# Optimization experiments

Hardware: AMD Instinct MI355X
Metric: run time of the kernel (lower is better)

## Reference

```python
import jax, jax.numpy as jnp
import numpy as np
import math

NUM_HEADS = 3
WINDOW = 7


def _shift_masks(ws):
    # row_mask: block mask for windows wrapping across the bottom edge
    half = ws * (ws // 2)  # 21 for ws=7
    row = np.zeros((ws * ws, ws * ws), np.float32)
    row[-half:, :-half] = -np.inf
    row[:-half, -half:] = -np.inf
    # column_mask = rearrange(row, '(r w1) (c w2) -> (w1 r) (w2 c)')
    col = row.reshape(ws, ws, ws, ws).transpose(1, 0, 3, 2).reshape(ws * ws, ws * ws)
    return jnp.asarray(row), jnp.asarray(col)


def setup_inputs() -> dict:
    key = jax.random.key(0)
    ks = jax.random.split(key, 5)
    B, S, E = 64, 3136, 96
    return {
        'x': jax.random.normal(ks[0], (B, S, E), jnp.float32),
        'w1': jax.random.normal(ks[1], (3 * E, E), jnp.float32) * 0.05,
        'b1': jax.random.normal(ks[2], (3 * E,), jnp.float32) * 0.05,
        'w2': jax.random.normal(ks[3], (E, E), jnp.float32) * 0.05,
        'b2': jax.random.normal(ks[4], (E,), jnp.float32) * 0.05,
    }


def reference(x, w1, b1, w2, b2):
    b, S, E = x.shape
    h = w = int(math.sqrt(S))          # 56
    ws = WINDOW
    H = NUM_HEADS
    Eh = E // H                        # head dim = 32
    nh, nw = h // ws, w // ws          # windows per axis = 8
    scale = 1.0 / math.sqrt(E / H)
    # faithful to original: forward shift = -ws//2 = -4, inverse shift = ws//2 = 3
    shift_fwd = -ws // 2
    shift_bwd = ws // 2

    qkv = x @ w1.T + b1                              # [b, S, 3E]
    qkv = qkv.reshape(b, h, w, E, 3)                 # (c K) split, K fastest
    qkv = jnp.roll(qkv, (shift_fwd, shift_fwd), axis=(1, 2))
    # b (nh m1) (nw m2) (H Eh) K -> b H nh nw (m1 m2) Eh K
    qkv = qkv.reshape(b, nh, ws, nw, ws, H, Eh, 3)
    qkv = qkv.transpose(0, 5, 1, 3, 2, 4, 6, 7).reshape(b, H, nh, nw, ws * ws, Eh, 3)
    Q, K, V = qkv[..., 0], qkv[..., 1], qkv[..., 2]

    s = jnp.einsum('bHhwme,bHhwne->bHhwmn', Q, K) * scale  # [b,H,nh,nw,49,49]
    row_mask, col_mask = _shift_masks(ws)
    s = s.at[:, :, -1, :].add(row_mask)   # last row of windows
    s = s.at[:, :, :, -1].add(col_mask)   # last column of windows

    att = jax.nn.softmax(s, axis=-1)
    o = jnp.einsum('bHhwmn,bHhwne->bHhwme', att, V)        # [b,H,nh,nw,49,Eh]
    # b H nh nw (m1 m2) Eh -> b (nh m1) (nw m2) (H Eh)
    o = o.reshape(b, H, nh, nw, ws, ws, Eh)
    o = o.transpose(0, 2, 4, 3, 5, 1, 6).reshape(b, h, w, E)
    o = jnp.roll(o, (shift_bwd, shift_bwd), axis=(1, 2))
    o = o.reshape(b, S, E)
    return o @ w2.T + b2
```

## Files before the change

### kernel.cpp

```cpp
#include <hip/hip_runtime.h>


typedef _Float16 f16;
typedef _Float16 f16x2 __attribute__((ext_vector_type(2)));
typedef _Float16 f16x4 __attribute__((ext_vector_type(4)));
typedef _Float16 f16x8 __attribute__((ext_vector_type(8)));
typedef float f32x4 __attribute__((ext_vector_type(4)));

static __device__ __forceinline__ f32x4 mfma16(f16x8 a, f16x8 b, f32x4 c) {
    return __builtin_amdgcn_mfma_f32_16x16x32_f16(a, b, c, 0, 0, 0);
}
static __device__ __forceinline__ f16x8 cvt8(const float* __restrict__ p) {
    float4 f0 = *(const float4*)(p);
    float4 f1 = *(const float4*)(p + 4);
    f16x8 h;
    h[0]=(f16)f0.x; h[1]=(f16)f0.y; h[2]=(f16)f0.z; h[3]=(f16)f0.w;
    h[4]=(f16)f1.x; h[5]=(f16)f1.y; h[6]=(f16)f1.z; h[7]=(f16)f1.w;
    return h;
}

#define SMEM_BYTES 31152
#define OFF_K  10192
#define OFF_VT 20384

union U2 { int i; f16x2 h; };
union U8 { int i[4]; f16x8 h; };

template<bool WS>
__global__ __launch_bounds__(256, 5) void swin_fused(
    const float* __restrict__ x, const float* __restrict__ w1,
    const float* __restrict__ b1, const float* __restrict__ w2,
    const float* __restrict__ b2, float* __restrict__ out,
    const f16* __restrict__ w1p, const f16* __restrict__ w2p,
    const float* __restrict__ b1p)
{
    __shared__ __align__(16) char smem[SMEM_BYTES];
    f16* q_s  = (f16*)(smem);
    f16* k_s  = (f16*)(smem + OFF_K);
    f16* vt_s = (f16*)(smem + OFF_VT);
    f16* o_s  = q_s;

    const int tid  = threadIdx.x;
    const int wv   = tid >> 6;
    const int lane = tid & 63;
    const int lrow = lane & 15;
    const int lq   = lane >> 4;

    const int bx = blockIdx.x;
    const int b  = bx >> 6;
    const int wz = bx & 63;
    const int wh = wz >> 3;
    const int ww = wz & 7;

    const float* xb = x + b * (3136 * 96);

    if (tid < 96) {
        #pragma unroll
        for (int p7 = 49; p7 < 56; ++p7) vt_s[tid * 56 + p7] = (f16)0.f;
    }
    if (tid < 8) vt_s[96 * 56 + tid] = (f16)0.f;

    {
        f16x8 bf[5][3];
        int   kq[5], cb[5];
        #pragma unroll
        for (int t = 0; t < 5; ++t) {
            int ot = wv + 4 * t;
            if (ot < 18) {
                int kqv = ot / 6;
                kq[t] = kqv;
                cb[t] = (ot - kqv * 6) * 16;
                if constexpr (WS) {
                    #pragma unroll
                    for (int ks = 0; ks < 3; ++ks)
                        bf[t][ks] = *(const f16x8*)(w1p + (ot*16 + lrow)*96 + ks*32 + lq*8);
                } else {
                    int srowA = (ot*16 + lrow - kqv*96) * 3 + kqv;
                    #pragma unroll
                    for (int ks = 0; ks < 3; ++ks)
                        bf[t][ks] = cvt8(w1 + srowA*96 + ks*32 + lq*8);
                }
            } else kq[t] = -1;
        }
        #pragma unroll
        for (int pt = 0; pt < 4; ++pt) {
            int p  = pt * 16 + lrow;
            int pc = (p < 49) ? p : 48;
            int i  = pc / 7, j = pc - i * 7;
            int r  = wh * 7 + i + 4; if (r >= 56) r -= 56;
            int c  = ww * 7 + j + 4; if (c >= 56) c -= 56;
            const float* xr = xb + (r * 56 + c) * 96;
            f16x8 xf[3];
            #pragma unroll
            for (int ks = 0; ks < 3; ++ks) xf[ks] = cvt8(xr + ks * 32 + lq * 8);
            const bool pok = (p < 49);
            #pragma unroll
            for (int t = 0; t < 5; ++t) {
                if (kq[t] < 0) continue;
                int ot = wv + 4 * t;
                f32x4 acc = {0.f, 0.f, 0.f, 0.f};
                if (kq[t] == 2) {
                    #pragma unroll
                    for (int ks = 0; ks < 3; ++ks) acc = mfma16(xf[ks], bf[t][ks], acc);
                    float bc;
                    if constexpr (WS) bc = b1p[ot*16 + lrow];
                    else              bc = b1[(ot*16 + lrow - 192)*3 + 2];
                    int cc = cb[t] + lrow;
                    f16x4 pk;
                    #pragma unroll
                    for (int i2 = 0; i2 < 4; ++i2) pk[i2] = (f16)(acc[i2] + bc);
                    int p4 = pt * 16 + lq * 4;
                    if (p4 < 45)       *(f16x4*)(vt_s + cc * 56 + p4) = pk;
                    else if (p4 == 48) vt_s[cc * 56 + 48] = pk[0];
                } else {
                    #pragma unroll
                    for (int ks = 0; ks < 3; ++ks) acc = mfma16(bf[t][ks], xf[ks], acc);
                    if (pok) {
                        f32x4 br;
                        if constexpr (WS) {
                            br = *(const f32x4*)(b1p + ot*16 + lq*4);
                        } else {
                            #pragma unroll
                            for (int i2 = 0; i2 < 4; ++i2)
                                br[i2] = b1[(ot*16 + lq*4 + i2 - kq[t]*96)*3 + kq[t]];
                        }
                        f16x4 pk;
                        #pragma unroll
                        for (int i2 = 0; i2 < 4; ++i2) pk[i2] = (f16)(acc[i2] + br[i2]);
                        f16* dst = (kq[t] == 0 ? q_s : k_s) + p * 104 + cb[t] + lq * 4;
                        *(f16x4*)dst = pk;
                    }
                }
            }
        }
    }
    __syncthreads();

    const bool mrow = (wh == 7), mcol = (ww == 7);
    const float scale = 0.17677669529663687f;
    const int m = wv * 16 + lrow;

    float mv[16];
    {
        const bool am = (m >= 28);
        const bool a4 = (m % 7) >= 4;
        #pragma unroll
        for (int nt = 0; nt < 4; ++nt)
            #pragma unroll
            for (int i2 = 0; i2 < 4; ++i2) {
                int nn = nt * 16 + lq * 4 + i2;
                bool ok = (nn < 49)
                       && (!mrow || (am == (nn >= 28)))
                       && (!mcol || (a4 == ((nn % 7) >= 4)));
                mv[nt*4 + i2] = ok ? 0.f : -3e38f;
            }
    }
    const int idxA = lrow + 32 * (lq & 1);
    const int idxB = idxA + 16;

    f16x8 bq[3];
    #pragma unroll
    for (int hh = 0; hh < 3; ++hh)
        bq[hh] = *(const f16x8*)(q_s + m * 104 + hh * 32 + lq * 8);

    #pragma unroll
    for (int hh = 0; hh < 3; ++hh) {
        f32x4 sc[4];
        #pragma unroll
        for (int nt = 0; nt < 4; ++nt) {
            f16x8 ak = *(const f16x8*)(k_s + (nt*16 + lrow)*104 + hh*32 + lq*8);
            f32x4 z = {0.f, 0.f, 0.f, 0.f};
            sc[nt] = mfma16(ak, bq[hh], z);
        }
        f16x8 va[2][2];
        #pragma unroll
        for (int et = 0; et < 2; ++et) {
            int vrow = hh * 32 + et * 16 + lrow;
            va[et][0] = *(const f16x8*)(vt_s + vrow * 56 + lq * 8);
            va[et][1] = *(const f16x8*)(vt_s + vrow * 56 + 32 + lq * 8);
        }
        float ev[16];
        #pragma unroll
        for (int nt = 0; nt < 4; ++nt)
            #pragma unroll
            for (int i2 = 0; i2 < 4; ++i2)
                ev[nt*4 + i2] = fmaf(sc[nt][i2], scale, mv[nt*4 + i2]);
        float tm[8];
        #pragma unroll
        for (int k2 = 0; k2 < 8; ++k2) tm[k2] = fmaxf(ev[2*k2], ev[2*k2+1]);
        #pragma unroll
        for (int k2 = 0; k2 < 4; ++k2) tm[k2] = fmaxf(tm[k2], tm[k2+4]);
        float vm = fmaxf(fmaxf(tm[0], tm[1]), fmaxf(tm[2], tm[3]));
        vm = fmaxf(vm, __shfl_xor(vm, 16));
        vm = fmaxf(vm, __shfl_xor(vm, 32));
        #pragma unroll
        for (int k2 = 0; k2 < 16; ++k2) ev[k2] = __expf(ev[k2] - vm);
        float ts[8];
        #pragma unroll
        for (int k2 = 0; k2 < 8; ++k2) ts[k2] = ev[2*k2] + ev[2*k2+1];
        #pragma unroll
        for (int k2 = 0; k2 < 4; ++k2) ts[k2] += ts[k2+4];
        float s = (ts[0] + ts[1]) + (ts[2] + ts[3]);
        s += __shfl_xor(s, 16);
        s += __shfl_xor(s, 32);
        float inv = 1.0f / s;

        int pd[4][2];
        #pragma unroll
        for (int nt = 0; nt < 4; ++nt) {
            U2 u0, u1;
            u0.h[0] = (f16)ev[nt*4+0]; u0.h[1] = (f16)ev[nt*4+1];
            u1.h[0] = (f16)ev[nt*4+2]; u1.h[1] = (f16)ev[nt*4+3];
            pd[nt][0] = u0.i; pd[nt][1] = u1.i;
        }
        U8 ub0, ub1;
        #pragma unroll
        for (int w = 0; w < 4; ++w) {
            int idx = (w < 2) ? idxA : idxB;
            int rr  = w & 1;
            int a0v = __shfl(pd[0][rr], idx);
            int a1v = __shfl(pd[1][rr], idx);
            ub0.i[w] = (lq & 2) ? a1v : a0v;
            int c0v = __shfl(pd[2][rr], idx);
            int c1v = __shfl(pd[3][rr], idx);
            ub1.i[w] = (lq & 2) ? c1v : c0v;
        }
        #pragma unroll
        for (int et = 0; et < 2; ++et) {
            f32x4 z = {0.f, 0.f, 0.f, 0.f};
            f32x4 oc = mfma16(va[et][0], ub0.h, z);
            oc = mfma16(va[et][1], ub1.h, oc);
            if (m < 49) {
                f16x4 pk;
                #pragma unroll
                for (int i2 = 0; i2 < 4; ++i2) pk[i2] = (f16)(oc[i2] * inv);
                *(f16x4*)(o_s + m * 104 + hh * 32 + et * 16 + lq * 4) = pk;
            }
        }
    }

    {
        f16x8 bo[3];
        #pragma unroll
        for (int ks = 0; ks < 3; ++ks)
            bo[ks] = *(const f16x8*)(o_s + m * 104 + ks * 32 + lq * 8);
        int mm2 = (m < 49) ? m : 48;
        int i = mm2 / 7, j = mm2 - i * 7;
        int orow = wh * 7 + i + 3; if (orow >= 56) orow -= 56;
        int ocol = ww * 7 + j + 3; if (ocol >= 56) ocol -= 56;
        float* op = out + (size_t)(b * 3136 + orow * 56 + ocol) * 96;
        #pragma unroll
        for (int ot2 = 0; ot2 < 6; ++ot2) {
            f32x4 acc = {0.f, 0.f, 0.f, 0.f};
            #pragma unroll
            for (int ks = 0; ks < 3; ++ks) {
                f16x8 aw;
                if constexpr (WS)
                    aw = *(const f16x8*)(w2p + (ot2*16 + lrow)*96 + ks*32 + lq*8);
                else
                    aw = cvt8(w2 + (ot2*16 + lrow)*96 + ks*32 + lq*8);
                acc = mfma16(aw, bo[ks], acc);
            }
            f32x4 bias = *(const f32x4*)(b2 + ot2 * 16 + lq * 4);
            if (m < 49) {
                f32x4 o4 = acc + bias;
                *(f32x4*)(op + ot2 * 16 + lq * 4) = o4;
            }
        }
    }
}

__global__ void prep_weights(const float* __restrict__ w1, const float* __restrict__ b1,
                             const float* __restrict__ w2,
                             f16* __restrict__ w1p, f16* __restrict__ w2p,
                             float* __restrict__ b1p)
{
    int idx = blockIdx.x * 256 + threadIdx.x;
    if (idx < 27648) {
        int np = idx / 96, k = idx - np * 96;
        int kq = np / 96, c96 = np - kq * 96;
        w1p[idx] = (f16)w1[(c96 * 3 + kq) * 96 + k];
    } else if (idx < 36864) {
        int i2 = idx - 27648;
        w2p[i2] = (f16)w2[i2];
    } else if (idx < 37152) {
        int np = idx - 36864;
        int kq = np / 96, c96 = np - kq * 96;
        b1p[np] = b1[c96 * 3 + kq];
    }
}

extern "C" void kernel_launch(void* const* d_in, const int* in_sizes, int n_in,
                              void* d_out, int out_size, void* d_ws, size_t ws_size,
                              hipStream_t stream) {
    const float* x  = (const float*)d_in[0];
    const float* w1 = (const float*)d_in[1];
    const float* b1 = (const float*)d_in[2];
    const float* w2 = (const float*)d_in[3];
    const float* b2 = (const float*)d_in[4];
    float* out = (float*)d_out;

    const size_t need = 27648u * 2 + 9216u * 2 + 288u * 4;
    if (ws_size >= need) {
        f16*   w1p = (f16*)d_ws;
        f16*   w2p = w1p + 27648;
        float* b1p = (float*)(w2p + 9216);
        prep_weights<<<dim3(146), dim3(256), 0, stream>>>(w1, b1, w2, w1p, w2p, b1p);
        swin_fused<true><<<dim3(4096), dim3(256), 0, stream>>>(
            x, w1, b1, w2, b2, out, w1p, w2p, b1p);
    } else {
        swin_fused<false><<<dim3(4096), dim3(256), 0, stream>>>(
            x, w1, b1, w2, b2, out, nullptr, nullptr, nullptr);
    }
}
```

Measured before the change: 258.9 us.

## Software-pipeline x, K and W2 loads with register double-buffering in fused Swin kernel

Adds register double-buffering in three phases. The x rows for the next pixel tile are prefetched while the current tile's QKV MFMAs run. The K fragments and QK^T scores for the next head are issued during the current head's softmax and PV. The W2 fragments for the next output tile are prefetched during the output projection. Launch bounds drop from 5 to 4 waves per SIMD to make room for the extra registers, which trades occupancy for instruction-level overlap.

```diff
diff --git a/kernel.cpp b/kernel.cpp
--- a/kernel.cpp
+++ b/kernel.cpp
@@ -18,6 +18,12 @@
     h[4]=(f16)f1.x; h[5]=(f16)f1.y; h[6]=(f16)f1.z; h[7]=(f16)f1.w;
     return h;
 }
+static __device__ __forceinline__ f16x8 cvt8p(const float4& f0, const float4& f1) {
+    f16x8 h;
+    h[0]=(f16)f0.x; h[1]=(f16)f0.y; h[2]=(f16)f0.z; h[3]=(f16)f0.w;
+    h[4]=(f16)f1.x; h[5]=(f16)f1.y; h[6]=(f16)f1.z; h[7]=(f16)f1.w;
+    return h;
+}
 
 #define SMEM_BYTES 31152
 #define OFF_K  10192
@@ -27,7 +33,7 @@
 union U8 { int i[4]; f16x8 h; };
 
 template<bool WS>
-__global__ __launch_bounds__(256, 5) void swin_fused(
+__global__ __launch_bounds__(256, 4) void swin_fused(
     const float* __restrict__ x, const float* __restrict__ w1,
     const float* __restrict__ b1, const float* __restrict__ w2,
     const float* __restrict__ b2, float* __restrict__ out,
@@ -82,6 +88,7 @@
                 }
             } else kq[t] = -1;
         }
+        const float* xrow[4];
         #pragma unroll
         for (int pt = 0; pt < 4; ++pt) {
             int p  = pt * 16 + lrow;
@@ -89,10 +96,29 @@
             int i  = pc / 7, j = pc - i * 7;
             int r  = wh * 7 + i + 4; if (r >= 56) r -= 56;
             int c  = ww * 7 + j + 4; if (c >= 56) c -= 56;
-            const float* xr = xb + (r * 56 + c) * 96;
+            xrow[pt] = xb + (r * 56 + c) * 96;
+        }
+        float4 xbuf0[3][2], xbuf1[3][2];
+        #pragma unroll
+        for (int ks = 0; ks < 3; ++ks) {
+            xbuf0[ks][0] = *(const float4*)(xrow[0] + ks * 32 + lq * 8);
+            xbuf0[ks][1] = *(const float4*)(xrow[0] + ks * 32 + lq * 8 + 4);
+        }
+        #pragma unroll
+        for (int pt = 0; pt < 4; ++pt) {
+            float4 (*cur)[2] = (pt & 1) ? xbuf1 : xbuf0;
+            float4 (*nxt)[2] = (pt & 1) ? xbuf0 : xbuf1;
+            if (pt < 3) {
+                #pragma unroll
+                for (int ks = 0; ks < 3; ++ks) {
+                    nxt[ks][0] = *(const float4*)(xrow[pt+1] + ks * 32 + lq * 8);
+                    nxt[ks][1] = *(const float4*)(xrow[pt+1] + ks * 32 + lq * 8 + 4);
+                }
+            }
             f16x8 xf[3];
             #pragma unroll
-            for (int ks = 0; ks < 3; ++ks) xf[ks] = cvt8(xr + ks * 32 + lq * 8);
+            for (int ks = 0; ks < 3; ++ks) xf[ks] = cvt8p(cur[ks][0], cur[ks][1]);
+            const int  p   = pt * 16 + lrow;
             const bool pok = (p < 49);
             #pragma unroll
             for (int t = 0; t < 5; ++t) {
@@ -163,14 +189,21 @@
     for (int hh = 0; hh < 3; ++hh)
         bq[hh] = *(const f16x8*)(q_s + m * 104 + hh * 32 + lq * 8);
 
+    f32x4 sc[4];
+    #pragma unroll
+    for (int nt = 0; nt < 4; ++nt) {
+        f16x8 ak = *(const f16x8*)(k_s + (nt*16 + lrow)*104 + lq*8);
+        f32x4 z = {0.f, 0.f, 0.f, 0.f};
+        sc[nt] = mfma16(ak, bq[0], z);
+    }
+
     #pragma unroll
     for (int hh = 0; hh < 3; ++hh) {
-        f32x4 sc[4];
-        #pragma unroll
-        for (int nt = 0; nt < 4; ++nt) {
-            f16x8 ak = *(const f16x8*)(k_s + (nt*16 + lrow)*104 + hh*32 + lq*8);
-            f32x4 z = {0.f, 0.f, 0.f, 0.f};
-            sc[nt] = mfma16(ak, bq[hh], z);
+        f16x8 akn[4];
+        if (hh < 2) {
+            #pragma unroll
+            for (int nt = 0; nt < 4; ++nt)
+                akn[nt] = *(const f16x8*)(k_s + (nt*16 + lrow)*104 + (hh+1)*32 + lq*8);
         }
         f16x8 va[2][2];
         #pragma unroll
@@ -237,6 +270,13 @@
                 *(f16x4*)(o_s + m * 104 + hh * 32 + et * 16 + lq * 4) = pk;
             }
         }
+        if (hh < 2) {
+            #pragma unroll
+            for (int nt = 0; nt < 4; ++nt) {
+                f32x4 z = {0.f, 0.f, 0.f, 0.f};
+                sc[nt] = mfma16(akn[nt], bq[hh+1], z);
+            }
+        }
     }
 
     {
@@ -249,18 +289,31 @@
         int orow = wh * 7 + i + 3; if (orow >= 56) orow -= 56;
         int ocol = ww * 7 + j + 3; if (ocol >= 56) ocol -= 56;
         float* op = out + (size_t)(b * 3136 + orow * 56 + ocol) * 96;
+
+        f16x8 aw0[3], aw1[3];
+        #pragma unroll
+        for (int ks = 0; ks < 3; ++ks) {
+            if constexpr (WS)
+                aw0[ks] = *(const f16x8*)(w2p + lrow*96 + ks*32 + lq*8);
+            else
+                aw0[ks] = cvt8(w2 + lrow*96 + ks*32 + lq*8);
+        }
         #pragma unroll
         for (int ot2 = 0; ot2 < 6; ++ot2) {
+            f16x8* cw = (ot2 & 1) ? aw1 : aw0;
+            f16x8* nw = (ot2 & 1) ? aw0 : aw1;
+            if (ot2 < 5) {
+                #pragma unroll
+                for (int ks = 0; ks < 3; ++ks) {
+                    if constexpr (WS)
+                        nw[ks] = *(const f16x8*)(w2p + ((ot2+1)*16 + lrow)*96 + ks*32 + lq*8);
+                    else
+                        nw[ks] = cvt8(w2 + ((ot2+1)*16 + lrow)*96 + ks*32 + lq*8);
+                }
+            }
             f32x4 acc = {0.f, 0.f, 0.f, 0.f};
             #pragma unroll
-            for (int ks = 0; ks < 3; ++ks) {
-                f16x8 aw;
-                if constexpr (WS)
-                    aw = *(const f16x8*)(w2p + (ot2*16 + lrow)*96 + ks*32 + lq*8);
-                else
-                    aw = cvt8(w2 + (ot2*16 + lrow)*96 + ks*32 + lq*8);
-                acc = mfma16(aw, bo[ks], acc);
-            }
+            for (int ks = 0; ks < 3; ++ks) acc = mfma16(cw[ks], bo[ks], acc);
             f32x4 bias = *(const f32x4*)(b2 + ot2 * 16 + lq * 4);
             if (m < 49) {
                 f32x4 o4 = acc + bias;
```

Result: faster. 238.4 us (-7.9%).
